# Optimization experiments

Hardware: AMD Instinct MI355X
Metric: run time of the kernel (lower is better)

Reference implementation:

```python
import jax, jax.numpy as jnp
import numpy as np

THRESHOLD = 0.5
PSI_ZONE = 0.1


def dequantize_ternary(w, threshold=THRESHOLD, psi_zone=PSI_ZONE):
    """Faithful reproduction of TernaryTensor.from_float followed by to_float.

    Branch order matches the original code:
      v > threshold        -> +1
      v < -threshold       -> -1
      |v| < psi_zone       -> 0
      otherwise (PSI)      -> (v + threshold) / (2 * threshold)  (stored psi_prob)
    """
    psi_val = (w + threshold) / (2.0 * threshold)
    return jnp.where(
        w > threshold, 1.0,
        jnp.where(
            w < -threshold, -1.0,
            jnp.where(jnp.abs(w) < psi_zone, 0.0, psi_val),
        ),
    ).astype(w.dtype)


def setup_inputs() -> dict:
    key = jax.random.key(0)
    k_x, k_w = jax.random.split(key)
    batch, in_features, out_features = 8192, 4096, 4096
    x = jax.random.normal(k_x, (batch, in_features), dtype=jnp.float32)
    # original: torch.randn(out, in) * 0.1
    weight_float = jax.random.normal(k_w, (out_features, in_features), dtype=jnp.float32) * 0.1
    bias = jnp.zeros((out_features,), dtype=jnp.float32)
    return {"x": x, "weight_float": weight_float, "bias": bias}


def reference(x, weight_float, bias):
    w = dequantize_ternary(weight_float)  # [out, in]
    return jnp.matmul(x, w.T) + bias      # [batch, out]
```

## Files before the change

kernel.cpp:

```cpp
#include <hip/hip_runtime.h>
#include <stdint.h>

#define THRESH 0.5f
#define PSI 0.1f

typedef short bfrag_t __attribute__((ext_vector_type(8)));
typedef float f32x16 __attribute__((ext_vector_type(16)));
typedef unsigned short u16x8 __attribute__((ext_vector_type(8)));

#define GLD16(gsrc, ldst)                                                                \
    __builtin_amdgcn_global_load_lds((const __attribute__((address_space(1))) void*)(gsrc), \
                                     (__attribute__((address_space(3))) void*)(ldst),       \
                                     16, 0, 0)

#define WAITVM(n) asm volatile("s_waitcnt vmcnt(" #n ")" ::: "memory")
#define WAITLGKM0() asm volatile("s_waitcnt lgkmcnt(0)" ::: "memory")
#define BAR()                                  \
    do {                                       \
        asm volatile("" ::: "memory");         \
        __builtin_amdgcn_s_barrier();          \
        asm volatile("" ::: "memory");         \
    } while (0)

__device__ __forceinline__ float dequant(float v) {
    if (v > THRESH) return 1.0f;
    if (v < -THRESH) return -1.0f;
    if (fabsf(v) < PSI) return 0.0f;
    return (v + THRESH) / (2.0f * THRESH);
}

__device__ __forceinline__ unsigned short f2bf(float f) {
    unsigned int u = __float_as_uint(f);
    u += 0x7FFFu + ((u >> 16) & 1u);
    return (unsigned short)(u >> 16);
}

template <bool DO_DEQUANT>
__global__ void pack_kernel(const float* __restrict__ src, unsigned short* __restrict__ dst, int K) {
    __shared__ char lsm[16384];
    const int t   = threadIdx.x;
    const int nkc = K >> 8;
    const int b   = blockIdx.x / nkc;
    const int kc  = blockIdx.x % nkc;
    const int k0  = kc << 8;
    const int r   = t >> 3;
    const int j   = t & 7;

    const float4* s4 = (const float4*)(src + (size_t)((b << 5) + r) * K + k0 + (j << 5));
    float4 f[8];
#pragma unroll
    for (int i = 0; i < 8; ++i) f[i] = s4[i];

#pragma unroll
    for (int gi = 0; gi < 4; ++gi) {
        float4 lo = f[2 * gi], hi4 = f[2 * gi + 1];
        u16x8 o;
        if (DO_DEQUANT) {
            o[0] = f2bf(dequant(lo.x));  o[1] = f2bf(dequant(lo.y));
            o[2] = f2bf(dequant(lo.z));  o[3] = f2bf(dequant(lo.w));
            o[4] = f2bf(dequant(hi4.x)); o[5] = f2bf(dequant(hi4.y));
            o[6] = f2bf(dequant(hi4.z)); o[7] = f2bf(dequant(hi4.w));
        } else {
            o[0] = f2bf(lo.x);  o[1] = f2bf(lo.y);  o[2] = f2bf(lo.z);  o[3] = f2bf(lo.w);
            o[4] = f2bf(hi4.x); o[5] = f2bf(hi4.y); o[6] = f2bf(hi4.z); o[7] = f2bf(hi4.w);
        }
        const int S_rel = 2 * j + (gi >> 1);
        const int slot  = ((gi & 1) << 5) + r;
        *(u16x8*)(lsm + S_rel * 1024 + slot * 16) = o;
    }
    __syncthreads();

    unsigned short* gdst = dst + (((size_t)b * (K >> 4) + (kc << 4)) << 9) + (size_t)t * 32;
#pragma unroll
    for (int i = 0; i < 4; ++i)
        *(u16x8*)(gdst + i * 8) = *(const u16x8*)(lsm + t * 64 + i * 16);
}


__device__ __forceinline__ bfrag_t rdfrag32(const char* halfBase, int band, int ks, int l16) {
    return *(const bfrag_t*)(halfBase + (band << 11) + (ks << 10) + l16);
}

__device__ __forceinline__ void mfma16(f32x16 (&acc)[4][2],
                                       const bfrag_t (&a)[4][2], const bfrag_t (&b)[2][2]) {
#pragma unroll
    for (int ks = 0; ks < 2; ++ks)
#pragma unroll
        for (int mi = 0; mi < 4; ++mi)
#pragma unroll
            for (int nn = 0; nn < 2; ++nn)
                acc[mi][nn] = __builtin_amdgcn_mfma_f32_32x32x16_bf16(
                    a[mi][ks], b[nn][ks], acc[mi][nn], 0, 0, 0);
}

__global__ __launch_bounds__(512, 2) void gemm256_kernel(
        const unsigned short* __restrict__ Ap,
        const unsigned short* __restrict__ Bp,
        const float* __restrict__ bias,
        float* __restrict__ C,
        int M, int N, int K) {
    __shared__ unsigned short lds[65536];
    char* ldsB = (char*)lds;

    const int t    = threadIdx.x;
    const int w    = t >> 6;
    const int l    = t & 63;
    const int wr   = w >> 2;
    const int wc   = w & 3;
    const int lr32 = l & 31;
    const int hi   = l >> 5;
    const int l16  = l << 4;

    const int nwg = gridDim.x;
    int bid = blockIdx.x;
    if ((nwg & 7) == 0) bid = (bid & 7) * (nwg >> 3) + (bid >> 3);
    const int nbn  = N >> 8;
    const int brow = (bid / nbn) << 8;
    const int bcol = (bid % nbn) << 8;

    const int Kc = K >> 4;
    const char* pA = (const char*)Ap + (((size_t)(((brow >> 5) + w) * (size_t)Kc)) << 10) + l16;
    const char* pB = (const char*)Bp + (((size_t)(((bcol >> 5) + w) * (size_t)Kc)) << 10) + l16;
    const int c16a = w * 2 + 0, c16b = w * 2 + 1;

#define STAGE_A(buf, half, kE)                                                              \
    do {                                                                                    \
        const size_t so_ = ((size_t)(((kE) >> 4) + (half) * 2)) << 10;                      \
        GLD16(pA + so_,        ldsB + (buf) * 65536 + (half) * 16384 + c16a * 1024);        \
        GLD16(pA + so_ + 1024, ldsB + (buf) * 65536 + (half) * 16384 + c16b * 1024);        \
    } while (0)
#define STAGE_B(buf, half, kE)                                                              \
    do {                                                                                    \
        const size_t so_ = ((size_t)(((kE) >> 4) + (half) * 2)) << 10;                      \
        GLD16(pB + so_,        ldsB + (buf) * 65536 + 32768 + (half) * 16384 + c16a * 1024);\
        GLD16(pB + so_ + 1024, ldsB + (buf) * 65536 + 32768 + (half) * 16384 + c16b * 1024);\
    } while (0)

    f32x16 acc[4][2];
#pragma unroll
    for (int m = 0; m < 4; ++m)
#pragma unroll
        for (int n = 0; n < 2; ++n)
#pragma unroll
            for (int r = 0; r < 16; ++r)
                acc[m][n][r] = 0.f;

    const int NT = K >> 6;
    const int wrB4 = wr << 2;
    const int wcB2 = wc << 1;
    const int wrBase = wr << 7;
    const int wcBase = wc << 6;

    {
        const int k1 = (NT > 1) ? 64 : 0;
        STAGE_A(0, 0, 0);  STAGE_B(0, 0, 0);  STAGE_A(0, 1, 0);  STAGE_B(0, 1, 0);
        STAGE_A(1, 0, k1); STAGE_B(1, 0, k1); STAGE_A(1, 1, k1); STAGE_B(1, 1, k1);
        WAITVM(8);
        BAR();
    }

    for (int tt = 0; tt < NT; ++tt) {
        const int X = tt & 1;
        const char* aH0 = ldsB + X * 65536;
        const char* aH1 = aH0 + 16384;
        const char* bH0 = aH0 + 32768;
        const char* bH1 = aH0 + 49152;
        int t2 = tt + 2; if (t2 >= NT) t2 -= NT;
        const int kX2 = t2 << 6;

        bfrag_t a0[4][2], b0[2][2], a1[4][2], b1[2][2];

#pragma unroll
        for (int mi = 0; mi < 4; ++mi)
#pragma unroll
            for (int ks = 0; ks < 2; ++ks)
                a0[mi][ks] = rdfrag32(aH0, wrB4 + mi, ks, l16);
#pragma unroll
        for (int nn = 0; nn < 2; ++nn)
#pragma unroll
            for (int ks = 0; ks < 2; ++ks)
                b0[nn][ks] = rdfrag32(bH0, wcB2 + nn, ks, l16);
#pragma unroll
        for (int nn = 0; nn < 2; ++nn)
#pragma unroll
            for (int ks = 0; ks < 2; ++ks)
                b1[nn][ks] = rdfrag32(bH1, wcB2 + nn, ks, l16);
#pragma unroll
        for (int mi = 0; mi < 4; ++mi)
#pragma unroll
            for (int ks = 0; ks < 2; ++ks)
                a1[mi][ks] = rdfrag32(aH1, wrB4 + mi, ks, l16);

        __builtin_amdgcn_s_setprio(1);
        mfma16(acc, a0, b0);
        __builtin_amdgcn_s_setprio(0);

        WAITLGKM0();
        BAR();

        STAGE_A(X, 0, kX2); STAGE_B(X, 0, kX2);
        STAGE_A(X, 1, kX2); STAGE_B(X, 1, kX2);

        __builtin_amdgcn_s_setprio(1);
        mfma16(acc, a1, b1);
        __builtin_amdgcn_s_setprio(0);

        WAITVM(8);
        BAR();
    }

    WAITVM(0);

    float bv[2];
#pragma unroll
    for (int nn = 0; nn < 2; ++nn) bv[nn] = bias[bcol + wcBase + nn * 32 + lr32];
#pragma unroll
    for (int mm = 0; mm < 4; ++mm) {
#pragma unroll
        for (int nn = 0; nn < 2; ++nn) {
            const int gc = bcol + wcBase + nn * 32 + lr32;
#pragma unroll
            for (int reg = 0; reg < 16; ++reg) {
                const int row = (reg & 3) + 8 * (reg >> 2) + 4 * hi;
                C[(size_t)(brow + wrBase + mm * 32 + row) * N + gc] = acc[mm][nn][reg] + bv[nn];
            }
        }
    }
    (void)M;
#undef STAGE_A
#undef STAGE_B
}

__global__ void gemm_fallback_kernel(const float* __restrict__ X, const float* __restrict__ W,
                                     const float* __restrict__ bias, float* __restrict__ C,
                                     int M, int N, int K) {
    __shared__ float sX[16][17];
    __shared__ float sW[16][17];
    const int tx = threadIdx.x & 15;
    const int ty = threadIdx.x >> 4;
    const int row = blockIdx.y * 16 + ty;
    const int colBase = blockIdx.x * 16;
    const int col = colBase + tx;
    float acc = 0.f;
    for (int k0 = 0; k0 < K; k0 += 16) {
        sX[ty][tx] = (row < M && k0 + tx < K) ? X[(size_t)row * K + k0 + tx] : 0.f;
        const int wrow = colBase + ty;
        sW[ty][tx] = (wrow < N && k0 + tx < K) ? dequant(W[(size_t)wrow * K + k0 + tx]) : 0.f;
        __syncthreads();
#pragma unroll
        for (int kk = 0; kk < 16; ++kk)
            acc += sX[ty][kk] * sW[tx][kk];
        __syncthreads();
    }
    if (row < M && col < N)
        C[(size_t)row * N + col] = acc + bias[col];
}

extern "C" void kernel_launch(void* const* d_in, const int* in_sizes, int n_in,
                              void* d_out, int out_size, void* d_ws, size_t ws_size,
                              hipStream_t stream) {
    const float* x    = (const float*)d_in[0];
    const float* w    = (const float*)d_in[1];
    const float* bias = (const float*)d_in[2];
    float* out        = (float*)d_out;

    const int N = in_sizes[2];
    const int K = in_sizes[1] / N;
    const int M = in_sizes[0] / K;

    const size_t need = ((size_t)M * K + (size_t)N * K) * sizeof(unsigned short);
    const bool fast = (ws_size >= need) && (M % 256 == 0) && (N % 256 == 0) &&
                      (K % 256 == 0);

    if (fast) {
        unsigned short* xp = (unsigned short*)d_ws;
        unsigned short* wp = xp + (size_t)M * K;
        pack_kernel<false><<<dim3((M / 32) * (K / 256)), dim3(256), 0, stream>>>(x, xp, K);
        pack_kernel<true ><<<dim3((N / 32) * (K / 256)), dim3(256), 0, stream>>>(w, wp, K);
        gemm256_kernel<<<dim3((M / 256) * (N / 256)), dim3(512), 0, stream>>>(xp, wp, bias, out, M, N, K);
    } else {
        dim3 g((N + 15) / 16, (M + 15) / 16);
        gemm_fallback_kernel<<<g, dim3(256), 0, stream>>>(x, w, bias, out, M, N, K);
    }
    (void)n_in; (void)out_size;
}
```

Measured before the change: 292.2 us.

## Switch GEMM to 256x128 tiles with K=32 stages and register double-buffered fragments

Replaces the 256x256 block tile (64 KB LDS, 2 blocks/CU) with a 256x128 tile, a K step of 32 and 48 KB LDS, targeting 4 blocks per CU. Each wave now computes a 64x64 sub-tile. The main loop is restructured to prefetch the next stage's fragments into an alternate register set while running MFMAs on the current one, with two barriers per step. The aim is higher occupancy and better latency hiding, at the cost of lower arithmetic intensity per block (more global and LDS traffic per FLOP) and more barriers.

```diff
diff --git a/kernel.cpp b/kernel.cpp
--- a/kernel.cpp
+++ b/kernel.cpp
@@ -77,36 +77,19 @@
 }
 
 
-__device__ __forceinline__ bfrag_t rdfrag32(const char* halfBase, int band, int ks, int l16) {
-    return *(const bfrag_t*)(halfBase + (band << 11) + (ks << 10) + l16);
-}
-
-__device__ __forceinline__ void mfma16(f32x16 (&acc)[4][2],
-                                       const bfrag_t (&a)[4][2], const bfrag_t (&b)[2][2]) {
-#pragma unroll
-    for (int ks = 0; ks < 2; ++ks)
-#pragma unroll
-        for (int mi = 0; mi < 4; ++mi)
-#pragma unroll
-            for (int nn = 0; nn < 2; ++nn)
-                acc[mi][nn] = __builtin_amdgcn_mfma_f32_32x32x16_bf16(
-                    a[mi][ks], b[nn][ks], acc[mi][nn], 0, 0, 0);
-}
-
-__global__ __launch_bounds__(512, 2) void gemm256_kernel(
+__global__ __launch_bounds__(512, 4) void gemm256x128_kernel(
         const unsigned short* __restrict__ Ap,
         const unsigned short* __restrict__ Bp,
         const float* __restrict__ bias,
         float* __restrict__ C,
         int M, int N, int K) {
-    __shared__ unsigned short lds[65536];
-    char* ldsB = (char*)lds;
+    __shared__ char ldsB[49152];
 
     const int t    = threadIdx.x;
     const int w    = t >> 6;
     const int l    = t & 63;
-    const int wr   = w >> 2;
-    const int wc   = w & 3;
+    const int wr   = w >> 1;
+    const int wc   = w & 1;
     const int lr32 = l & 31;
     const int hi   = l >> 5;
     const int l16  = l << 4;
@@ -114,121 +97,104 @@
     const int nwg = gridDim.x;
     int bid = blockIdx.x;
     if ((nwg & 7) == 0) bid = (bid & 7) * (nwg >> 3) + (bid >> 3);
-    const int nbn  = N >> 8;
+    const int nbn  = N >> 7;
     const int brow = (bid / nbn) << 8;
-    const int bcol = (bid % nbn) << 8;
+    const int bcol = (bid % nbn) << 7;
 
     const int Kc = K >> 4;
-    const char* pA = (const char*)Ap + (((size_t)(((brow >> 5) + w) * (size_t)Kc)) << 10) + l16;
-    const char* pB = (const char*)Bp + (((size_t)(((bcol >> 5) + w) * (size_t)Kc)) << 10) + l16;
-    const int c16a = w * 2 + 0, c16b = w * 2 + 1;
-
-#define STAGE_A(buf, half, kE)                                                              \
-    do {                                                                                    \
-        const size_t so_ = ((size_t)(((kE) >> 4) + (half) * 2)) << 10;                      \
-        GLD16(pA + so_,        ldsB + (buf) * 65536 + (half) * 16384 + c16a * 1024);        \
-        GLD16(pA + so_ + 1024, ldsB + (buf) * 65536 + (half) * 16384 + c16b * 1024);        \
-    } while (0)
-#define STAGE_B(buf, half, kE)                                                              \
-    do {                                                                                    \
-        const size_t so_ = ((size_t)(((kE) >> 4) + (half) * 2)) << 10;                      \
-        GLD16(pB + so_,        ldsB + (buf) * 65536 + 32768 + (half) * 16384 + c16a * 1024);\
-        GLD16(pB + so_ + 1024, ldsB + (buf) * 65536 + 32768 + (half) * 16384 + c16b * 1024);\
-    } while (0)
-
-    f32x16 acc[4][2];
-#pragma unroll
-    for (int m = 0; m < 4; ++m)
+    const char* pA = (const char*)Ap + (((size_t)((brow >> 5) + w)        * (size_t)Kc) << 10) + l16;
+    const char* pB = (const char*)Bp + (((size_t)((bcol >> 5) + (w >> 1)) * (size_t)Kc) << 10) + l16;
+    const int wpar = w & 1;
+
+#define STAGE(i2, BO)                                                                     \
+    do {                                                                                  \
+        const size_t sa_ = (size_t)(i2) << 11;                                            \
+        GLD16(pA + sa_,        ldsB + (BO) + (w << 11));                                  \
+        GLD16(pA + sa_ + 1024, ldsB + (BO) + (w << 11) + 1024);                           \
+        GLD16(pB + ((size_t)(((i2) << 1) + wpar) << 10), ldsB + (BO) + 16384 + (w << 10));\
+    } while (0)
+
+#define READF(BO, Af, Bf)                                                                 \
+    do {                                                                                  \
+        _Pragma("unroll") for (int mi = 0; mi < 2; ++mi)                                  \
+        _Pragma("unroll") for (int ks = 0; ks < 2; ++ks)                                  \
+            Af[mi][ks] = *(const bfrag_t*)(ldsB + (BO) +                                  \
+                (((((wr << 1) + mi) << 1) | ks) << 10) + l16);                            \
+        _Pragma("unroll") for (int nn = 0; nn < 2; ++nn)                                  \
+        _Pragma("unroll") for (int ks = 0; ks < 2; ++ks)                                  \
+            Bf[nn][ks] = *(const bfrag_t*)(ldsB + (BO) + 16384 +                          \
+                (((((wc << 1) + nn) << 1) | ks) << 10) + l16);                            \
+    } while (0)
+
+#define MFMA8(Af, Bf)                                                                     \
+    do {                                                                                  \
+        __builtin_amdgcn_s_setprio(1);                                                    \
+        _Pragma("unroll") for (int ks = 0; ks < 2; ++ks)                                  \
+        _Pragma("unroll") for (int mi = 0; mi < 2; ++mi)                                  \
+        _Pragma("unroll") for (int nn = 0; nn < 2; ++nn)                                  \
+            acc[mi][nn] = __builtin_amdgcn_mfma_f32_32x32x16_bf16(                        \
+                Af[mi][ks], Bf[nn][ks], acc[mi][nn], 0, 0, 0);                            \
+        __builtin_amdgcn_s_setprio(0);                                                    \
+    } while (0)
+
+#define BODY(i, XO, YO, Aalt, Balt, Acur, Bcur)                                           \
+    do {                                                                                  \
+        int i2_ = (i) + 2; if (i2_ >= NT) i2_ -= NT;     \
+        WAITLGKM0();                                            \
+        BAR();                                    \
+        STAGE(i2_, XO);                                                                   \
+        WAITVM(3);                       \
+        BAR();                                                \
+        READF(YO, Aalt, Balt);              \
+        MFMA8(Acur, Bcur);                                                                \
+    } while (0)
+
+    f32x16 acc[2][2];
+#pragma unroll
+    for (int m = 0; m < 2; ++m)
 #pragma unroll
         for (int n = 0; n < 2; ++n)
 #pragma unroll
             for (int r = 0; r < 16; ++r)
                 acc[m][n][r] = 0.f;
 
-    const int NT = K >> 6;
-    const int wrB4 = wr << 2;
-    const int wcB2 = wc << 1;
-    const int wrBase = wr << 7;
-    const int wcBase = wc << 6;
-
-    {
-        const int k1 = (NT > 1) ? 64 : 0;
-        STAGE_A(0, 0, 0);  STAGE_B(0, 0, 0);  STAGE_A(0, 1, 0);  STAGE_B(0, 1, 0);
-        STAGE_A(1, 0, k1); STAGE_B(1, 0, k1); STAGE_A(1, 1, k1); STAGE_B(1, 1, k1);
-        WAITVM(8);
-        BAR();
-    }
-
-    for (int tt = 0; tt < NT; ++tt) {
-        const int X = tt & 1;
-        const char* aH0 = ldsB + X * 65536;
-        const char* aH1 = aH0 + 16384;
-        const char* bH0 = aH0 + 32768;
-        const char* bH1 = aH0 + 49152;
-        int t2 = tt + 2; if (t2 >= NT) t2 -= NT;
-        const int kX2 = t2 << 6;
-
-        bfrag_t a0[4][2], b0[2][2], a1[4][2], b1[2][2];
-
-#pragma unroll
-        for (int mi = 0; mi < 4; ++mi)
-#pragma unroll
-            for (int ks = 0; ks < 2; ++ks)
-                a0[mi][ks] = rdfrag32(aH0, wrB4 + mi, ks, l16);
-#pragma unroll
-        for (int nn = 0; nn < 2; ++nn)
-#pragma unroll
-            for (int ks = 0; ks < 2; ++ks)
-                b0[nn][ks] = rdfrag32(bH0, wcB2 + nn, ks, l16);
-#pragma unroll
-        for (int nn = 0; nn < 2; ++nn)
-#pragma unroll
-            for (int ks = 0; ks < 2; ++ks)
-                b1[nn][ks] = rdfrag32(bH1, wcB2 + nn, ks, l16);
-#pragma unroll
-        for (int mi = 0; mi < 4; ++mi)
-#pragma unroll
-            for (int ks = 0; ks < 2; ++ks)
-                a1[mi][ks] = rdfrag32(aH1, wrB4 + mi, ks, l16);
-
-        __builtin_amdgcn_s_setprio(1);
-        mfma16(acc, a0, b0);
-        __builtin_amdgcn_s_setprio(0);
-
-        WAITLGKM0();
-        BAR();
-
-        STAGE_A(X, 0, kX2); STAGE_B(X, 0, kX2);
-        STAGE_A(X, 1, kX2); STAGE_B(X, 1, kX2);
-
-        __builtin_amdgcn_s_setprio(1);
-        mfma16(acc, a1, b1);
-        __builtin_amdgcn_s_setprio(0);
-
-        WAITVM(8);
-        BAR();
+    const int NT = K >> 5;
+
+    bfrag_t aA[2][2], bA[2][2], aB[2][2], bB[2][2];
+
+    STAGE(0, 0);
+    STAGE(1, 24576);
+    WAITVM(3);
+    BAR();
+    READF(0, aA, bA);
+
+    for (int i = 0; i < NT; i += 2) {
+        BODY(i,     0,     24576, aB, bB, aA, bA);
+        BODY(i + 1, 24576, 0,     aA, bA, aB, bB);
     }
 
     WAITVM(0);
 
     float bv[2];
 #pragma unroll
-    for (int nn = 0; nn < 2; ++nn) bv[nn] = bias[bcol + wcBase + nn * 32 + lr32];
-#pragma unroll
-    for (int mm = 0; mm < 4; ++mm) {
+    for (int nn = 0; nn < 2; ++nn) bv[nn] = bias[bcol + (wc << 6) + nn * 32 + lr32];
+#pragma unroll
+    for (int mm = 0; mm < 2; ++mm) {
 #pragma unroll
         for (int nn = 0; nn < 2; ++nn) {
-            const int gc = bcol + wcBase + nn * 32 + lr32;
+            const int gc = bcol + (wc << 6) + nn * 32 + lr32;
 #pragma unroll
             for (int reg = 0; reg < 16; ++reg) {
                 const int row = (reg & 3) + 8 * (reg >> 2) + 4 * hi;
-                C[(size_t)(brow + wrBase + mm * 32 + row) * N + gc] = acc[mm][nn][reg] + bv[nn];
+                C[(size_t)(brow + (wr << 6) + mm * 32 + row) * N + gc] = acc[mm][nn][reg] + bv[nn];
             }
         }
     }
     (void)M;
-#undef STAGE_A
-#undef STAGE_B
+#undef STAGE
+#undef READF
+#undef MFMA8
+#undef BODY
 }
 
 __global__ void gemm_fallback_kernel(const float* __restrict__ X, const float* __restrict__ W,
@@ -269,7 +235,7 @@
     const int M = in_sizes[0] / K;
 
     const size_t need = ((size_t)M * K + (size_t)N * K) * sizeof(unsigned short);
-    const bool fast = (ws_size >= need) && (M % 256 == 0) && (N % 256 == 0) &&
+    const bool fast = (ws_size >= need) && (M % 256 == 0) && (N % 128 == 0) &&
                       (K % 256 == 0);
 
     if (fast) {
@@ -277,7 +243,7 @@
         unsigned short* wp = xp + (size_t)M * K;
         pack_kernel<false><<<dim3((M / 32) * (K / 256)), dim3(256), 0, stream>>>(x, xp, K);
         pack_kernel<true ><<<dim3((N / 32) * (K / 256)), dim3(256), 0, stream>>>(w, wp, K);
-        gemm256_kernel<<<dim3((M / 256) * (N / 256)), dim3(512), 0, stream>>>(xp, wp, bias, out, M, N, K);
+        gemm256x128_kernel<<<dim3((M / 256) * (N / 128)), dim3(512), 0, stream>>>(xp, wp, bias, out, M, N, K);
     } else {
         dim3 g((N + 15) / 16, (M + 15) / 16);
         gemm_fallback_kernel<<<g, dim3(256), 0, stream>>>(x, w, bias, out, M, N, K);
```

Result: slower. 817.7 us (+179.8%).

## Restructure GEMM main loop into quadrant-split MFMA with interleaved A/B staging

Applied to the files above, without the earlier changes.

Rewrites the GEMM inner loop so each 64-wide K tile is processed in two M-quadrant halves with finer-grained lgkmcnt waits and sched barriers, staging A for the next tile and B for the tile after into alternating buffers. The aim is to overlap LDS fragment reads and global-to-LDS loads with MFMA issue, and to cut register pressure by holding only half the A fragments at once. The loop is unrolled by two to alternate buffers statically. Splitting the A and B prefetch distances makes the synchronisation harder to get right, and the extra barriers add stall points.

```diff
diff --git a/kernel.cpp b/kernel.cpp
--- a/kernel.cpp
+++ b/kernel.cpp
@@ -13,8 +13,9 @@
                                      (__attribute__((address_space(3))) void*)(ldst),       \
                                      16, 0, 0)
 
-#define WAITVM(n) asm volatile("s_waitcnt vmcnt(" #n ")" ::: "memory")
-#define WAITLGKM0() asm volatile("s_waitcnt lgkmcnt(0)" ::: "memory")
+#define WAITVM(n)   asm volatile("s_waitcnt vmcnt(" #n ")" ::: "memory")
+#define WAITLGKM(n) asm volatile("s_waitcnt lgkmcnt(" #n ")" ::: "memory")
+#define SB()        __builtin_amdgcn_sched_barrier(0)
 #define BAR()                                  \
     do {                                       \
         asm volatile("" ::: "memory");         \
@@ -81,26 +82,13 @@
     return *(const bfrag_t*)(halfBase + (band << 11) + (ks << 10) + l16);
 }
 
-__device__ __forceinline__ void mfma16(f32x16 (&acc)[4][2],
-                                       const bfrag_t (&a)[4][2], const bfrag_t (&b)[2][2]) {
-#pragma unroll
-    for (int ks = 0; ks < 2; ++ks)
-#pragma unroll
-        for (int mi = 0; mi < 4; ++mi)
-#pragma unroll
-            for (int nn = 0; nn < 2; ++nn)
-                acc[mi][nn] = __builtin_amdgcn_mfma_f32_32x32x16_bf16(
-                    a[mi][ks], b[nn][ks], acc[mi][nn], 0, 0, 0);
-}
-
-__global__ __launch_bounds__(512, 2) void gemm256_kernel(
+__global__ __launch_bounds__(512, 2) void gemm256p_kernel(
         const unsigned short* __restrict__ Ap,
         const unsigned short* __restrict__ Bp,
         const float* __restrict__ bias,
         float* __restrict__ C,
         int M, int N, int K) {
-    __shared__ unsigned short lds[65536];
-    char* ldsB = (char*)lds;
+    __shared__ char ldsB[131072];
 
     const int t    = threadIdx.x;
     const int w    = t >> 6;
@@ -136,6 +124,16 @@
         GLD16(pB + so_ + 1024, ldsB + (buf) * 65536 + 32768 + (half) * 16384 + c16b * 1024);\
     } while (0)
 
+#define QMFMA(qm, bq, nn)                                                                 \
+    do {                                                                                  \
+        __builtin_amdgcn_s_setprio(1);                                                    \
+        _Pragma("unroll") for (int ks = 0; ks < 4; ++ks)                                  \
+        _Pragma("unroll") for (int mi = 0; mi < 2; ++mi)                                  \
+            acc[(qm) * 2 + mi][nn] = __builtin_amdgcn_mfma_f32_32x32x16_bf16(             \
+                a[mi][ks], bq[ks], acc[(qm) * 2 + mi][nn], 0, 0, 0);                      \
+        __builtin_amdgcn_s_setprio(0);                                                    \
+    } while (0)
+
     f32x16 acc[4][2];
 #pragma unroll
     for (int m = 0; m < 4; ++m)
@@ -148,87 +146,81 @@
     const int NT = K >> 6;
     const int wrB4 = wr << 2;
     const int wcB2 = wc << 1;
-    const int wrBase = wr << 7;
-    const int wcBase = wc << 6;
-
-    {
-        const int k1 = (NT > 1) ? 64 : 0;
-        STAGE_A(0, 0, 0);  STAGE_B(0, 0, 0);  STAGE_A(0, 1, 0);  STAGE_B(0, 1, 0);
-        STAGE_A(1, 0, k1); STAGE_B(1, 0, k1); STAGE_A(1, 1, k1); STAGE_B(1, 1, k1);
-        WAITVM(8);
-        BAR();
-    }
-
-    for (int tt = 0; tt < NT; ++tt) {
-        const int X = tt & 1;
-        const char* aH0 = ldsB + X * 65536;
-        const char* aH1 = aH0 + 16384;
-        const char* bH0 = aH0 + 32768;
-        const char* bH1 = aH0 + 49152;
-        int t2 = tt + 2; if (t2 >= NT) t2 -= NT;
-        const int kX2 = t2 << 6;
-
-        bfrag_t a0[4][2], b0[2][2], a1[4][2], b1[2][2];
-
-#pragma unroll
-        for (int mi = 0; mi < 4; ++mi)
-#pragma unroll
-            for (int ks = 0; ks < 2; ++ks)
-                a0[mi][ks] = rdfrag32(aH0, wrB4 + mi, ks, l16);
-#pragma unroll
-        for (int nn = 0; nn < 2; ++nn)
-#pragma unroll
-            for (int ks = 0; ks < 2; ++ks)
-                b0[nn][ks] = rdfrag32(bH0, wcB2 + nn, ks, l16);
-#pragma unroll
-        for (int nn = 0; nn < 2; ++nn)
-#pragma unroll
-            for (int ks = 0; ks < 2; ++ks)
-                b1[nn][ks] = rdfrag32(bH1, wcB2 + nn, ks, l16);
-#pragma unroll
-        for (int mi = 0; mi < 4; ++mi)
-#pragma unroll
-            for (int ks = 0; ks < 2; ++ks)
-                a1[mi][ks] = rdfrag32(aH1, wrB4 + mi, ks, l16);
-
-        __builtin_amdgcn_s_setprio(1);
-        mfma16(acc, a0, b0);
-        __builtin_amdgcn_s_setprio(0);
-
-        WAITLGKM0();
-        BAR();
-
-        STAGE_A(X, 0, kX2); STAGE_B(X, 0, kX2);
-        STAGE_A(X, 1, kX2); STAGE_B(X, 1, kX2);
-
-        __builtin_amdgcn_s_setprio(1);
-        mfma16(acc, a1, b1);
-        __builtin_amdgcn_s_setprio(0);
-
-        WAITVM(8);
-        BAR();
+
+    STAGE_A(0, 0, 0);  STAGE_A(0, 1, 0);
+    STAGE_B(0, 0, 0);  STAGE_B(0, 1, 0);
+    STAGE_B(1, 0, 64); STAGE_B(1, 1, 64);
+    WAITVM(4);
+    BAR();
+
+    bfrag_t a[2][4], b0[4], b1[4];
+
+#define TILE(tv, XO, YO, Xb, Yb)                                                          \
+    do {                                                                                  \
+        int t1_ = (tv) + 1; if (t1_ >= NT) t1_ -= NT;              \
+        int t2_ = (tv) + 2; if (t2_ >= NT) t2_ -= NT;                                     \
+        const char* aH0 = ldsB + (XO);                                                    \
+        const char* aH1 = aH0 + 16384;                                                    \
+        const char* bH0 = aH0 + 32768;                                                    \
+        const char* bH1 = aH0 + 49152;                                                    \
+        const int kY1 = t1_ << 6, kX2 = t2_ << 6;                                         \
+                                                \
+        _Pragma("unroll") for (int mi = 0; mi < 2; ++mi)                                  \
+        _Pragma("unroll") for (int ks = 0; ks < 4; ++ks)                                  \
+            a[mi][ks] = rdfrag32(ks < 2 ? aH0 : aH1, wrB4 + mi, ks & 1, l16);             \
+        _Pragma("unroll") for (int ks = 0; ks < 4; ++ks)                                  \
+            b0[ks] = rdfrag32(ks < 2 ? bH0 : bH1, wcB2 + 0, ks & 1, l16);                 \
+        SB();                                                                             \
+                                                                  \
+        _Pragma("unroll") for (int ks = 0; ks < 4; ++ks)                                  \
+            b1[ks] = rdfrag32(ks < 2 ? bH0 : bH1, wcB2 + 1, ks & 1, l16);                 \
+        SB();                                                                             \
+        STAGE_A(Yb, 0, kY1); STAGE_A(Yb, 1, kY1);                                         \
+        WAITLGKM(4); SB();                          \
+        QMFMA(0, b0, 0);                                                                  \
+        WAITLGKM(0); SB();                                                   \
+        QMFMA(0, b1, 1);                                                                  \
+                              \
+        _Pragma("unroll") for (int mi = 0; mi < 2; ++mi)                                  \
+        _Pragma("unroll") for (int ks = 0; ks < 4; ++ks)                                  \
+            a[mi][ks] = rdfrag32(ks < 2 ? aH0 : aH1, wrB4 + 2 + mi, ks & 1, l16);         \
+        SB();                                                                             \
+        BAR();                        \
+        STAGE_B(Xb, 0, kX2); STAGE_B(Xb, 1, kX2);                                         \
+        WAITLGKM(0); SB();                                              \
+        QMFMA(1, b1, 1);                                                                  \
+        QMFMA(1, b0, 0);                                                                  \
+        WAITVM(4);                            \
+        BAR();                                                             \
+    } while (0)
+
+    for (int tt = 0; tt < NT; tt += 2) {
+        TILE(tt,     0,     65536, 0, 1);
+        TILE(tt + 1, 65536, 0,     1, 0);
     }
 
     WAITVM(0);
 
     float bv[2];
 #pragma unroll
-    for (int nn = 0; nn < 2; ++nn) bv[nn] = bias[bcol + wcBase + nn * 32 + lr32];
+    for (int nn = 0; nn < 2; ++nn) bv[nn] = bias[bcol + (wc << 6) + nn * 32 + lr32];
 #pragma unroll
     for (int mm = 0; mm < 4; ++mm) {
 #pragma unroll
         for (int nn = 0; nn < 2; ++nn) {
-            const int gc = bcol + wcBase + nn * 32 + lr32;
+            const int gc = bcol + (wc << 6) + nn * 32 + lr32;
 #pragma unroll
             for (int reg = 0; reg < 16; ++reg) {
                 const int row = (reg & 3) + 8 * (reg >> 2) + 4 * hi;
-                C[(size_t)(brow + wrBase + mm * 32 + row) * N + gc] = acc[mm][nn][reg] + bv[nn];
+                C[(size_t)(brow + (wr << 7) + mm * 32 + row) * N + gc] = acc[mm][nn][reg] + bv[nn];
             }
         }
     }
     (void)M;
 #undef STAGE_A
 #undef STAGE_B
+#undef QMFMA
+#undef TILE
 }
 
 __global__ void gemm_fallback_kernel(const float* __restrict__ X, const float* __restrict__ W,
@@ -277,7 +269,7 @@
         unsigned short* wp = xp + (size_t)M * K;
         pack_kernel<false><<<dim3((M / 32) * (K / 256)), dim3(256), 0, stream>>>(x, xp, K);
         pack_kernel<true ><<<dim3((N / 32) * (K / 256)), dim3(256), 0, stream>>>(w, wp, K);
-        gemm256_kernel<<<dim3((M / 256) * (N / 256)), dim3(512), 0, stream>>>(xp, wp, bias, out, M, N, K);
+        gemm256p_kernel<<<dim3((M / 256) * (N / 256)), dim3(512), 0, stream>>>(xp, wp, bias, out, M, N, K);
     } else {
         dim3 g((N + 15) / 16, (M + 15) / 16);
         gemm_fallback_kernel<<<g, dim3(256), 0, stream>>>(x, w, bias, out, M, N, K);
```

Measured after the change: 301.0 us. 3.0% more time.
